# Optimization experiments

Hardware: AMD Instinct MI355X
Metric: run time of the kernel (lower is better)

The kernel has to match this reference:

```python
import jax, jax.numpy as jnp
import numpy as np

D = 256
H = 8
HD = D // H  # 32
EPS = 1e-5


def _ln(x, g, b):
    m = jnp.mean(x, axis=-1, keepdims=True)
    v = jnp.var(x, axis=-1, keepdims=True)
    return (x - m) * jax.lax.rsqrt(v + EPS) * g + b


def setup_inputs() -> dict:
    key = jax.random.key(0)
    ks = jax.random.split(key, 30)
    B = 131072
    s = 0.05

    def w(k, shape, scale=s):
        return jax.random.normal(k, shape, dtype=jnp.float32) * scale

    inp = {
        'f24': w(ks[0], (B, D), 1.0),
        'f77': w(ks[1], (B, D), 1.0),
        'fx': w(ks[2], (B, D), 1.0),
        'norm_g': jnp.ones((D,), jnp.float32),
        'norm_b': jnp.zeros((D,), jnp.float32),
        'Wq24': w(ks[3], (D, D)), 'bq24': w(ks[4], (D,)),
        'Wk24': w(ks[5], (D, D)), 'bk24': w(ks[6], (D,)),
        'Wv24': w(ks[7], (D, D)), 'bv24': w(ks[8], (D,)),
        'Wq77': w(ks[9], (D, D)), 'bq77': w(ks[10], (D,)),
        'Wk77': w(ks[11], (D, D)), 'bk77': w(ks[12], (D,)),
        'Wv77': w(ks[13], (D, D)), 'bv77': w(ks[14], (D,)),
        'Wqx': w(ks[15], (D, D)), 'bqx': w(ks[16], (D,)),
        'Wkx': w(ks[17], (D, D)), 'bkx': w(ks[18], (D,)),
        'Wvx': w(ks[19], (D, D)), 'bvx': w(ks[20], (D,)),
        'Wout': w(ks[21], (D, D)), 'bout': w(ks[22], (D,)),
        'radar_w': jnp.ones((3,), jnp.float32),
        'W1': w(ks[23], (D, 4 * D)), 'b1': w(ks[24], (4 * D,)),
        'W2': w(ks[25], (4 * D, D)), 'b2': w(ks[26], (D,)),
        'fnorm_g': jnp.ones((D,), jnp.float32),
        'fnorm_b': jnp.zeros((D,), jnp.float32),
    }
    return inp


def reference(f24, f77, fx, norm_g, norm_b,
              Wq24, bq24, Wk24, bk24, Wv24, bv24,
              Wq77, bq77, Wk77, bk77, Wv77, bv77,
              Wqx, bqx, Wkx, bkx, Wvx, bvx,
              Wout, bout, radar_w, W1, b1, W2, b2,
              fnorm_g, fnorm_b):
    B = f24.shape[0]
    residual = (f24 + f77 + fx) / 3.0
    n24 = _ln(f24, norm_g, norm_b)
    n77 = _ln(f77, norm_g, norm_b)
    nx = _ln(fx, norm_g, norm_b)

    def proj(x, W, b):
        return (x @ W + b).reshape(B, H, HD)

    q24 = proj(n24, Wq24, bq24); k24 = proj(n24, Wk24, bk24); v24 = proj(n24, Wv24, bv24)
    q77 = proj(n77, Wq77, bq77); k77 = proj(n77, Wk77, bk77); v77 = proj(n77, Wv77, bv77)
    qx = proj(nx, Wqx, bqx); kx = proj(nx, Wkx, bkx); vx = proj(nx, Wvx, bvx)

    scale = HD ** (-0.5)

    def att(q, ka, kb):  # [B,H,H] each
        a = jnp.einsum('bhd,bgd->bhg', q, ka) * scale
        b_ = jnp.einsum('bhd,bgd->bhg', q, kb) * scale
        # softmax across the two radar sources (stacked dim), NOT over keys
        return jax.nn.softmax(jnp.stack([a, b_], axis=1), axis=1)

    attn_24 = att(q24, k77, kx)
    attn_77 = att(q77, k24, kx)
    attn_x = att(qx, k24, k77)

    def mix(p, va, vb):  # [B,2,H,H] x [B,H,HD] -> [B, D]
        o = jnp.einsum('bhg,bgd->bhd', p[:, 0], va) + jnp.einsum('bhg,bgd->bhd', p[:, 1], vb)
        return o.reshape(B, D)

    out_24 = mix(attn_24, v77, vx)
    out_77 = mix(attn_77, v24, vx)
    out_x = mix(attn_x, v24, v77)

    rw = jax.nn.softmax(radar_w, axis=0)
    fused = rw[0] * out_24 + rw[1] * out_77 + rw[2] * out_x
    fused = fused @ Wout + bout
    fused = fused + residual
    ff = jax.nn.gelu(fused @ W1 + b1, approximate=False) @ W2 + b2  # dropout = eval identity
    output = _ln(fused + ff, fnorm_g, fnorm_b)
    return output, rw
```

## Files before the change

kernel.cpp:

```cpp
#include <hip/hip_runtime.h>

#define DEV __device__ __forceinline__

typedef float f4_t __attribute__((ext_vector_type(4)));
typedef short v8s  __attribute__((ext_vector_type(8)));

DEV float lo16(unsigned int w){ return __uint_as_float(w << 16); }
DEV float hi16(unsigned int w){ return __uint_as_float(w & 0xffff0000u); }
DEV float b2f(unsigned short u){ return __uint_as_float((unsigned)u << 16); }
DEV unsigned short f2b(float f){
  unsigned int x = __float_as_uint(f);
  x += 0x7fffu + ((x >> 16) & 1u);
  return (unsigned short)(x >> 16);
}
DEV float geluf(float v){ return 0.5f * v * (1.0f + erff(v * 0.7071067811865475f)); }

DEV void gload_lds16(const unsigned short* g, unsigned short* l){
  __builtin_amdgcn_global_load_lds(
      (const __attribute__((address_space(1))) void*)g,
      (__attribute__((address_space(3))) void*)l, 16, 0, 0);
}

#define WAITV(n) asm volatile("s_waitcnt vmcnt(" #n ")" ::: "memory")
#define SBAR()  do{ __builtin_amdgcn_sched_barrier(0); \
                    asm volatile("s_barrier" ::: "memory"); \
                    __builtin_amdgcn_sched_barrier(0); }while(0)

__global__ void k_prep(
    const float* Wq24, const float* Wk24, const float* Wv24,
    const float* Wq77, const float* Wk77, const float* Wv77,
    const float* Wqx,  const float* Wkx,  const float* Wvx,
    const float* bq24, const float* bk24, const float* bv24,
    const float* bq77, const float* bk77, const float* bv77,
    const float* bqx,  const float* bkx,  const float* bvx,
    const float* Wout, const float* W1,   const float* W2,
    const float* radar_w,
    unsigned short* wt_cat, unsigned short* wout_t,
    unsigned short* w1_t, unsigned short* w2_t,
    float* bias_cat, float* rwbuf, float* out_tail)
{
  long idx = (long)blockIdx.x * blockDim.x + threadIdx.x;
  if (idx < 589824){
    int s = (int)(idx / 196608);
    int r = (int)(idx % 196608);
    int ng = r >> 8, k = r & 255;
    int which = ng >> 8, n = ng & 255;
    const float* src;
    switch (s*3 + which){
      case 0: src = Wq24; break;  case 1: src = Wk24; break;  case 2: src = Wv24; break;
      case 3: src = Wq77; break;  case 4: src = Wk77; break;  case 5: src = Wv77; break;
      case 6: src = Wqx;  break;  case 7: src = Wkx;  break;  default: src = Wvx; break;
    }
    wt_cat[idx] = f2b(src[k*256 + n]);
    return;
  }
  idx -= 589824;
  if (idx < 65536){ int n = (int)(idx >> 8), k = (int)(idx & 255);
    wout_t[idx] = f2b(Wout[k*256 + n]); return; }
  idx -= 65536;
  if (idx < 262144){ int n = (int)(idx >> 8), k = (int)(idx & 255);
    w1_t[idx] = f2b(W1[k*1024 + n]); return; }
  idx -= 262144;
  if (idx < 262144){ int n = (int)(idx >> 10), k = (int)(idx & 1023);
    w2_t[idx] = f2b(W2[k*256 + n]); return; }
  idx -= 262144;
  if (idx < 2304){
    int s = (int)(idx / 768), j = (int)(idx % 768);
    int which = j >> 8, jj = j & 255;
    const float* src;
    switch (s*3 + which){
      case 0: src = bq24; break;  case 1: src = bk24; break;  case 2: src = bv24; break;
      case 3: src = bq77; break;  case 4: src = bk77; break;  case 5: src = bv77; break;
      case 6: src = bqx;  break;  case 7: src = bkx;  break;  default: src = bvx; break;
    }
    bias_cat[idx] = src[jj]; return;
  }
  idx -= 2304;
  if (idx < 3){
    float w0 = radar_w[0], w1v = radar_w[1], w2v = radar_w[2];
    float m = fmaxf(w0, fmaxf(w1v, w2v));
    float e0 = __expf(w0-m), e1 = __expf(w1v-m), e2 = __expf(w2v-m);
    float inv = 1.0f/(e0+e1+e2);
    float rw = (idx==0 ? e0 : (idx==1 ? e1 : e2)) * inv;
    rwbuf[idx] = rw; out_tail[idx] = rw;
  }
}

__global__ __launch_bounds__(256) void k_ln3(
    const float* __restrict__ f24, const float* __restrict__ f77, const float* __restrict__ fx,
    const float* __restrict__ gg, const float* __restrict__ bb,
    unsigned short* __restrict__ nbuf, float* __restrict__ resid, int rows)
{
  int wid = threadIdx.x >> 6, lane = threadIdx.x & 63;
  long row = (long)blockIdx.x*4 + wid;
  long base = row*256 + lane*4;
  f4_t x0 = *(const f4_t*)(f24 + base);
  f4_t x1 = *(const f4_t*)(f77 + base);
  f4_t x2 = *(const f4_t*)(fx  + base);
  float s[3], q[3];
  s[0]=x0.x+x0.y+x0.z+x0.w;
  s[1]=x1.x+x1.y+x1.z+x1.w;
  s[2]=x2.x+x2.y+x2.z+x2.w;
  q[0]=fmaf(x0.x,x0.x,fmaf(x0.y,x0.y,fmaf(x0.z,x0.z,x0.w*x0.w)));
  q[1]=fmaf(x1.x,x1.x,fmaf(x1.y,x1.y,fmaf(x1.z,x1.z,x1.w*x1.w)));
  q[2]=fmaf(x2.x,x2.x,fmaf(x2.y,x2.y,fmaf(x2.z,x2.z,x2.w*x2.w)));
  #pragma unroll
  for (int m=1;m<64;m<<=1){
    #pragma unroll
    for (int j=0;j<3;j++){ s[j]+=__shfl_xor(s[j],m); q[j]+=__shfl_xor(q[j],m); }
  }
  f4_t G  = *(const f4_t*)(gg + lane*4);
  f4_t Bv = *(const f4_t*)(bb + lane*4);
  long strm = (long)rows*256;
  {
    float mean = s[0]*(1.0f/256.0f);
    float rstd = rsqrtf(q[0]*(1.0f/256.0f) - mean*mean + 1e-5f);
    ushort4 o;
    o.x=f2b((x0.x-mean)*rstd*G.x+Bv.x); o.y=f2b((x0.y-mean)*rstd*G.y+Bv.y);
    o.z=f2b((x0.z-mean)*rstd*G.z+Bv.z); o.w=f2b((x0.w-mean)*rstd*G.w+Bv.w);
    *(ushort4*)(nbuf + base) = o;
  }
  {
    float mean = s[1]*(1.0f/256.0f);
    float rstd = rsqrtf(q[1]*(1.0f/256.0f) - mean*mean + 1e-5f);
    ushort4 o;
    o.x=f2b((x1.x-mean)*rstd*G.x+Bv.x); o.y=f2b((x1.y-mean)*rstd*G.y+Bv.y);
    o.z=f2b((x1.z-mean)*rstd*G.z+Bv.z); o.w=f2b((x1.w-mean)*rstd*G.w+Bv.w);
    *(ushort4*)(nbuf + strm + base) = o;
  }
  {
    float mean = s[2]*(1.0f/256.0f);
    float rstd = rsqrtf(q[2]*(1.0f/256.0f) - mean*mean + 1e-5f);
    ushort4 o;
    o.x=f2b((x2.x-mean)*rstd*G.x+Bv.x); o.y=f2b((x2.y-mean)*rstd*G.y+Bv.y);
    o.z=f2b((x2.z-mean)*rstd*G.z+Bv.z); o.w=f2b((x2.w-mean)*rstd*G.w+Bv.w);
    *(ushort4*)(nbuf + 2*strm + base) = o;
  }
  f4_t rs;
  rs.x=(x0.x+x1.x+x2.x)*(1.0f/3.0f);
  rs.y=(x0.y+x1.y+x2.y)*(1.0f/3.0f);
  rs.z=(x0.z+x1.z+x2.z)*(1.0f/3.0f);
  rs.w=(x0.w+x1.w+x2.w)*(1.0f/3.0f);
  *(f4_t*)(resid + base) = rs;
}

template<int EPI>
__global__ __launch_bounds__(256,2) void k_gemm256(
    const unsigned short* __restrict__ A, const unsigned short* __restrict__ Bt,
    const float* __restrict__ bias, const float* __restrict__ resid,
    unsigned short* __restrict__ outH,
    long aBatch, long bBatch, long biasBatch, long oBatch, int ldOut,
    int tM, int tN, int tZ)
{
  __shared__ __align__(16) unsigned short As[2][128][64];
  __shared__ __align__(16) unsigned short Bs[2][128][64];
  int tid = threadIdx.x, wid = tid >> 6, lane = tid & 63;
  int wm = (wid >> 1)*64, wn = (wid & 1)*64;
  int lr = lane & 15, lk = lane >> 4;

  int total = tM*tN*tZ;
  int nT = (total - (int)blockIdx.x + (int)gridDim.x - 1) / (int)gridDim.x;
  if (nT <= 0) return;
  int G = nT*4;

  auto tileOf = [&](int j, long& m0, int& n0, int& z){
    int T = (int)blockIdx.x + j*(int)gridDim.x;
    int mt = T % tM; int rest = T / tM;
    int nt = rest % tN; z = rest / tN;
    m0 = (long)mt*128; n0 = nt*128;
  };

  auto stage = [&](int g){
    long m0; int n0, z;
    tileOf(g >> 2, m0, n0, z);
    int k0 = (g & 3)*64, bi = g & 1;
    const unsigned short* Ab = A  + (long)z*aBatch + m0*256;
    const unsigned short* Bb = Bt + (long)z*bBatch + (long)n0*256;
    #pragma unroll
    for (int i=0;i<4;i++){
      int c = (wid*4+i)*64 + lane;
      int r = c >> 3, sl = (c & 7) ^ (r & 7);
      gload_lds16(Ab + (long)r*256 + k0 + sl*8, &As[bi][0][0] + (long)(wid*4+i)*512);
      gload_lds16(Bb + (long)r*256 + k0 + sl*8, &Bs[bi][0][0] + (long)(wid*4+i)*512);
    }
  };

  const f4_t fz = {0.f,0.f,0.f,0.f};
  f4_t acc[4][4] = {};

  stage(0);
  for (int g=0; g<G; ++g){
    if (g+1 < G){ stage(g+1); WAITV(8); }
    else        { WAITV(0); }
    SBAR();
    int cur = g & 1;
    #pragma unroll
    for (int ks=0; ks<2; ++ks){
      v8s af[4], bfv[4];
      #pragma unroll
      for (int f=0; f<4; f++){
        int prA = wm + f*16 + lr;
        int prB = wn + f*16 + lr;
        int js  = ks*4 + lk;
        af[f]  = *(const v8s*)&As[cur][prA][(js ^ (prA & 7))*8];
        bfv[f] = *(const v8s*)&Bs[cur][prB][(js ^ (prB & 7))*8];
      }
      #pragma unroll
      for (int fm=0; fm<4; fm++)
        #pragma unroll
        for (int fn=0; fn<4; fn++)
          acc[fm][fn] = __builtin_amdgcn_mfma_f32_16x16x32_bf16(bfv[fn], af[fm], acc[fm][fn], 0,0,0);
    }
    if ((g & 3) == 3){
      long m0; int n0, z;
      tileOf(g >> 2, m0, n0, z);
      long zo = (long)z*oBatch;
      const float* bp = bias + (long)z*biasBatch;
      #pragma unroll
      for (int fm=0; fm<4; fm++){
        long gm = m0 + wm + fm*16 + lr;
        long rowo = zo + gm*(long)ldOut;
        #pragma unroll
        for (int fn=0; fn<4; fn++){
          int gn = n0 + wn + fn*16 + lk*4;
          f4_t bv = *(const f4_t*)(bp + gn);
          f4_t v = acc[fm][fn];
          v.x += bv.x; v.y += bv.y; v.z += bv.z; v.w += bv.w;
          if (EPI == 1){
            f4_t rv = *(const f4_t*)(resid + rowo + gn);
            v.x += rv.x; v.y += rv.y; v.z += rv.z; v.w += rv.w;
          }
          if (EPI == 2){ v.x=geluf(v.x); v.y=geluf(v.y); v.z=geluf(v.z); v.w=geluf(v.w); }
          ushort4 o; o.x=f2b(v.x); o.y=f2b(v.y); o.z=f2b(v.z); o.w=f2b(v.w);
          *(ushort4*)(outH + rowo + gn) = o;
          acc[fm][fn] = fz;
        }
      }
    }
    SBAR();
  }
}

__global__ __launch_bounds__(512,4) void k_attn(
    const unsigned short* __restrict__ qkv, const float* __restrict__ rwb,
    unsigned short* __restrict__ outA, int rows)
{
  __shared__ __align__(16) unsigned short L[8][72][40];
  int tid = threadIdx.x, wid = tid >> 6, lane = tid & 63;
  long brow0 = (long)blockIdx.x * 8;
  for (int c = tid; c < 2304; c += 512){
    int row = c / 288, rem = c % 288;
    int s = rem / 96, cc = rem % 96;
    int vi = cc >> 2, ch = cc & 3;
    const uint4* src = (const uint4*)(qkv + ((long)s*rows + brow0 + row)*768 + cc*8);
    *(uint4*)&L[row][s*24 + vi][ch*8] = *src;
  }
  __syncthreads();

  int h = lane >> 3, g = lane & 7;
  const unsigned short* R = &L[wid][0][0];
  float comb[32];
  #pragma unroll
  for (int i=0;i<32;i++) comb[i] = 0.0f;
  float rw0 = rwb[0], rw1 = rwb[1], rw2 = rwb[2];

  #pragma unroll
  for (int att=0; att<3; ++att){
    int qs  = att;
    int as_ = (att==0) ? 1 : 0;
    int bs_ = (att==2) ? 1 : 2;
    float rwv = (att==0) ? rw0 : ((att==1) ? rw1 : rw2);
    const unsigned short* qp  = R + (qs *24      + h)*40;
    const unsigned short* kap = R + (as_*24 + 8  + g)*40;
    const unsigned short* kbp = R + (bs_*24 + 8  + g)*40;
    float a = 0.0f, b = 0.0f;
    #pragma unroll
    for (int j=0;j<4;j++){
      uint4 qc  = *(const uint4*)(qp  + j*8);
      uint4 kac = *(const uint4*)(kap + j*8);
      uint4 kbc = *(const uint4*)(kbp + j*8);
      #define DOT2(QW,KA,KB) { float q0=lo16(QW), q1=hi16(QW); \
        a=fmaf(q0,lo16(KA),a); a=fmaf(q1,hi16(KA),a); \
        b=fmaf(q0,lo16(KB),b); b=fmaf(q1,hi16(KB),b); }
      DOT2(qc.x, kac.x, kbc.x) DOT2(qc.y, kac.y, kbc.y)
      DOT2(qc.z, kac.z, kbc.z) DOT2(qc.w, kac.w, kbc.w)
      #undef DOT2
    }
    float d  = (b - a) * 0.17677669529663689f;
    float p0 = 1.0f / (1.0f + __expf(d));
    float p1 = 1.0f - p0;
    float w0 = rwv * p0, w1 = rwv * p1;
    const unsigned short* vap = R + (as_*24 + 16 + g)*40;
    const unsigned short* vbp = R + (bs_*24 + 16 + g)*40;
    #pragma unroll
    for (int j=0;j<4;j++){
      uint4 va = *(const uint4*)(vap + j*8);
      uint4 vb = *(const uint4*)(vbp + j*8);
      #define MIX2(VA,VB,C0,C1) { \
        C0 = fmaf(w0, lo16(VA), fmaf(w1, lo16(VB), C0)); \
        C1 = fmaf(w0, hi16(VA), fmaf(w1, hi16(VB), C1)); }
      MIX2(va.x, vb.x, comb[j*8+0], comb[j*8+1])
      MIX2(va.y, vb.y, comb[j*8+2], comb[j*8+3])
      MIX2(va.z, vb.z, comb[j*8+4], comb[j*8+5])
      MIX2(va.w, vb.w, comb[j*8+6], comb[j*8+7])
      #undef MIX2
    }
  }

  float t16[16];
  { bool up = (lane & 4) != 0;
    #pragma unroll
    for (int i=0;i<16;i++){
      float send = up ? comb[i] : comb[16+i];
      float keep = up ? comb[16+i] : comb[i];
      t16[i] = keep + __shfl_xor(send, 4);
    } }
  float t8[8];
  { bool up = (lane & 2) != 0;
    #pragma unroll
    for (int i=0;i<8;i++){
      float send = up ? t16[i] : t16[8+i];
      float keep = up ? t16[8+i] : t16[i];
      t8[i] = keep + __shfl_xor(send, 2);
    } }
  float t4[4];
  { bool up = (lane & 1) != 0;
    #pragma unroll
    for (int i=0;i<4;i++){
      float send = up ? t8[i] : t8[4+i];
      float keep = up ? t8[4+i] : t8[i];
      t4[i] = keep + __shfl_xor(send, 1);
    } }

  long orow = brow0 + wid;
  ushort4 o4;
  o4.x = f2b(t4[0]); o4.y = f2b(t4[1]); o4.z = f2b(t4[2]); o4.w = f2b(t4[3]);
  *(ushort4*)(outA + orow*256 + lane*4) = o4;
}

__global__ __launch_bounds__(512,4) void k_ff2ln(
    const unsigned short* __restrict__ A, const unsigned short* __restrict__ Bt,
    const float* __restrict__ b2, const unsigned short* __restrict__ fusedH,
    const float* __restrict__ fg, const float* __restrict__ fb,
    float* __restrict__ dout)
{
  __shared__ __align__(16) union {
    struct { unsigned short As[2][64][64]; unsigned short Bs[2][256][64]; } st;
    float rowbuf[64][264];
  } u;
  int tid = threadIdx.x, wid = tid >> 6, lane = tid & 63;
  long m0 = (long)blockIdx.x * 64;
  const unsigned short* Ab = A + m0*1024;

  auto stage = [&](int it){
    int k0 = (it)*64, bi = it & 1;
    { int c = wid*64 + lane; int r = c >> 3, sl = (c & 7) ^ (r & 7);
      gload_lds16(Ab + (long)r*1024 + k0 + sl*8, &u.st.As[bi][0][0] + (long)wid*512); }
    #pragma unroll
    for (int i=0;i<4;i++){
      int j = wid*4 + i; int c = j*64 + lane; int r = c >> 3, sl = (c & 7) ^ (r & 7);
      gload_lds16(Bt + (long)r*1024 + k0 + sl*8, &u.st.Bs[bi][0][0] + (long)j*512);
    }
  };

  f4_t acc[2][4] = {};
  int wm = (wid >> 2)*32, wn = (wid & 3)*64;
  int lr = lane & 15, lk = lane >> 4;

  stage(0);
  for (int it=0; it<16; ++it){
    if (it+1 < 16){ stage(it+1); WAITV(5); }
    else          { WAITV(0); }
    SBAR();
    int cur = it & 1;
    #pragma unroll
    for (int ks=0; ks<2; ++ks){
      v8s af[2], bfv[4];
      #pragma unroll
      for (int f=0; f<2; f++){
        int pr = wm + f*16 + lr;
        af[f]  = *(const v8s*)&u.st.As[cur][pr][((ks*4+lk) ^ (pr & 7))*8];
      }
      #pragma unroll
      for (int f=0; f<4; f++){
        int pr = wn + f*16 + lr;
        bfv[f] = *(const v8s*)&u.st.Bs[cur][pr][((ks*4+lk) ^ (pr & 7))*8];
      }
      #pragma unroll
      for (int fm=0; fm<2; fm++)
        #pragma unroll
        for (int fn=0; fn<4; fn++)
          acc[fm][fn] = __builtin_amdgcn_mfma_f32_16x16x32_bf16(bfv[fn], af[fm], acc[fm][fn], 0,0,0);
    }
    SBAR();
  }

  #pragma unroll
  for (int fm=0; fm<2; fm++){
    int rl = wm + fm*16 + lr;
    #pragma unroll
    for (int fn=0; fn<4; fn++){
      int cl = wn + fn*16 + lk*4;
      f4_t bv = *(const f4_t*)(b2 + cl);
      ushort4 fh = *(const ushort4*)(fusedH + (m0 + rl)*256 + cl);
      f4_t v = acc[fm][fn];
      v.x += bv.x + b2f(fh.x);
      v.y += bv.y + b2f(fh.y);
      v.z += bv.z + b2f(fh.z);
      v.w += bv.w + b2f(fh.w);
      *(f4_t*)&u.rowbuf[rl][cl] = v;
    }
  }
  __syncthreads();

  f4_t G  = *(const f4_t*)(fg + lane*4);
  f4_t Bv = *(const f4_t*)(fb + lane*4);
  #pragma unroll
  for (int rr=0; rr<8; ++rr){
    int row = wid*8 + rr;
    f4_t x = *(const f4_t*)&u.rowbuf[row][lane*4];
    float s = x.x + x.y + x.z + x.w;
    float q = fmaf(x.x,x.x, fmaf(x.y,x.y, fmaf(x.z,x.z, x.w*x.w)));
    #pragma unroll
    for (int m=1;m<64;m<<=1){ s += __shfl_xor(s,m); q += __shfl_xor(q,m); }
    float mean = s*(1.0f/256.0f);
    float rstd = rsqrtf(q*(1.0f/256.0f) - mean*mean + 1e-5f);
    f4_t o;
    o.x = (x.x-mean)*rstd*G.x + Bv.x;
    o.y = (x.y-mean)*rstd*G.y + Bv.y;
    o.z = (x.z-mean)*rstd*G.z + Bv.z;
    o.w = (x.w-mean)*rstd*G.w + Bv.w;
    *(f4_t*)(dout + (m0 + row)*256 + lane*4) = o;
  }
}

extern "C" void kernel_launch(void* const* d_in, const int* in_sizes, int n_in,
                              void* d_out, int out_size, void* d_ws, size_t ws_size,
                              hipStream_t stream)
{
  const float* f24    = (const float*)d_in[0];
  const float* f77    = (const float*)d_in[1];
  const float* fx     = (const float*)d_in[2];
  const float* norm_g = (const float*)d_in[3];
  const float* norm_b = (const float*)d_in[4];
  const float* Wq24 = (const float*)d_in[5];  const float* bq24 = (const float*)d_in[6];
  const float* Wk24 = (const float*)d_in[7];  const float* bk24 = (const float*)d_in[8];
  const float* Wv24 = (const float*)d_in[9];  const float* bv24 = (const float*)d_in[10];
  const float* Wq77 = (const float*)d_in[11]; const float* bq77 = (const float*)d_in[12];
  const float* Wk77 = (const float*)d_in[13]; const float* bk77 = (const float*)d_in[14];
  const float* Wv77 = (const float*)d_in[15]; const float* bv77 = (const float*)d_in[16];
  const float* Wqx  = (const float*)d_in[17]; const float* bqx  = (const float*)d_in[18];
  const float* Wkx  = (const float*)d_in[19]; const float* bkx  = (const float*)d_in[20];
  const float* Wvx  = (const float*)d_in[21]; const float* bvx  = (const float*)d_in[22];
  const float* Wout = (const float*)d_in[23]; const float* bout = (const float*)d_in[24];
  const float* radar_w = (const float*)d_in[25];
  const float* W1 = (const float*)d_in[26];   const float* b1 = (const float*)d_in[27];
  const float* W2 = (const float*)d_in[28];   const float* b2 = (const float*)d_in[29];
  const float* fnorm_g = (const float*)d_in[30];
  const float* fnorm_b = (const float*)d_in[31];

  const long Brows = (long)in_sizes[0] / 256;
  float* dout = (float*)d_out;
  char* ws = (char*)d_ws;

  size_t off = 0;
  auto A_ = [&](size_t b){ size_t o = off; off = (off + b + 255) & ~(size_t)255; return o; };
  size_t oWT = A_((size_t)3*768*256*2);
  size_t oWO = A_((size_t)65536*2);
  size_t oW1 = A_((size_t)262144*2);
  size_t oW2 = A_((size_t)262144*2);
  size_t oBC = A_((size_t)2304*4);
  size_t oRW = A_(256);
  size_t fixedEnd = off;

  unsigned short* WT_CAT = (unsigned short*)(ws + oWT);
  unsigned short* WOUT_T = (unsigned short*)(ws + oWO);
  unsigned short* W1_T   = (unsigned short*)(ws + oW1);
  unsigned short* W2_T   = (unsigned short*)(ws + oW2);
  float*          BIASC  = (float*)(ws + oBC);
  float*          RW     = (float*)(ws + oRW);

  const size_t PER_ROW = 7168;
  if (ws_size <= fixedEnd + 512) return;
  long maxR = (long)((ws_size - fixedEnd - 256) / PER_ROW);
  maxR &= ~127L;
  if (maxR < 128) return;
  long Rc = maxR < 16384 ? maxR : 16384;
  if (Rc > Brows) Rc = Brows;
  long nch = (Brows + Rc - 1) / Rc;
  Rc = ((Brows + nch - 1) / nch + 127) & ~127L;

  size_t chunkBase = (fixedEnd + 255) & ~(size_t)255;
  char* NB_B = ws + chunkBase;
  char* RS_B = NB_B + (size_t)1536*Rc;
  char* QK_B = RS_B + (size_t)1024*Rc;

  {
    long total = 589824 + 65536 + 262144 + 262144 + 2304 + 3;
    int blocks = (int)((total + 255) / 256);
    k_prep<<<blocks, 256, 0, stream>>>(
        Wq24, Wk24, Wv24, Wq77, Wk77, Wv77, Wqx, Wkx, Wvx,
        bq24, bk24, bv24, bq77, bk77, bv77, bqx, bkx, bvx,
        Wout, W1, W2, radar_w,
        WT_CAT, WOUT_T, W1_T, W2_T, BIASC, RW, dout + (size_t)Brows*256);
  }

  for (long row0 = 0; row0 < Brows; row0 += Rc){
    long rows = Brows - row0 < Rc ? Brows - row0 : Rc;
    unsigned short* NBUF   = (unsigned short*)NB_B;
    float*          RESID  = (float*)RS_B;
    unsigned short* QKV    = (unsigned short*)QK_B;
    unsigned short* ATTN   = (unsigned short*)NB_B;
    unsigned short* FUSEDH = (unsigned short*)QK_B;
    unsigned short* HBUF   = (unsigned short*)(QK_B + (size_t)rows*256*2);

    int tM = (int)(rows/128);

    k_ln3<<<(int)(rows/4), 256, 0, stream>>>(
        f24 + row0*256, f77 + row0*256, fx + row0*256,
        norm_g, norm_b, NBUF, RESID, (int)rows);

    { int tiles = tM*6*3; int grid = tiles < 512 ? tiles : 512;
      k_gemm256<0><<<grid, 256, 0, stream>>>(
          NBUF, WT_CAT, BIASC, nullptr, QKV,
          rows*256L, 768L*256, 768L, rows*768L, 768, tM, 6, 3); }

    k_attn<<<(int)(rows/8), 512, 0, stream>>>(QKV, RW, ATTN, (int)rows);

    { int tiles = tM*2; int grid = tiles < 512 ? tiles : 512;
      k_gemm256<1><<<grid, 256, 0, stream>>>(
          ATTN, WOUT_T, bout, RESID, FUSEDH,
          0, 0, 0, 0, 256, tM, 2, 1); }

    { int tiles = tM*8; int grid = tiles < 512 ? tiles : 512;
      k_gemm256<2><<<grid, 256, 0, stream>>>(
          FUSEDH, W1_T, b1, nullptr, HBUF,
          0, 0, 0, 0, 1024, tM, 8, 1); }

    k_ff2ln<<<(int)(rows/64), 512, 0, stream>>>(
        HBUF, W2_T, b2, FUSEDH, fnorm_g, fnorm_b, dout + row0*256);
  }
}
```

Baseline: 1.445 ms.

## Replace persistent GEMM tile loop with one-tile-per-block grid and shrink attention blocks

The GEMM kernel no longer loops persistently over tiles with cross-tile prefetch. Each block now computes a single 128x128 tile from a 3D grid, with the bias hoisted ahead of the K loop and the 4-step K loop fully unrolled. The attention kernel moves from 512-thread blocks handling 8 rows to 256-thread blocks handling 4 rows, with a higher occupancy hint. This cuts index arithmetic and lets the hardware scheduler balance work across CUs, but it gives up prefetching the next tile during the epilogue and adds launch overhead from many more blocks.

After: 1.989 ms. 1.38x slower.

```diff
diff --git a/kernel.cpp b/kernel.cpp
--- a/kernel.cpp
+++ b/kernel.cpp
@@ -149,33 +149,21 @@
     const unsigned short* __restrict__ A, const unsigned short* __restrict__ Bt,
     const float* __restrict__ bias, const float* __restrict__ resid,
     unsigned short* __restrict__ outH,
-    long aBatch, long bBatch, long biasBatch, long oBatch, int ldOut,
-    int tM, int tN, int tZ)
+    long aBatch, long bBatch, long biasBatch, long oBatch, int ldOut)
 {
   __shared__ __align__(16) unsigned short As[2][128][64];
   __shared__ __align__(16) unsigned short Bs[2][128][64];
   int tid = threadIdx.x, wid = tid >> 6, lane = tid & 63;
   int wm = (wid >> 1)*64, wn = (wid & 1)*64;
   int lr = lane & 15, lk = lane >> 4;
-
-  int total = tM*tN*tZ;
-  int nT = (total - (int)blockIdx.x + (int)gridDim.x - 1) / (int)gridDim.x;
-  if (nT <= 0) return;
-  int G = nT*4;
-
-  auto tileOf = [&](int j, long& m0, int& n0, int& z){
-    int T = (int)blockIdx.x + j*(int)gridDim.x;
-    int mt = T % tM; int rest = T / tM;
-    int nt = rest % tN; z = rest / tN;
-    m0 = (long)mt*128; n0 = nt*128;
-  };
-
-  auto stage = [&](int g){
-    long m0; int n0, z;
-    tileOf(g >> 2, m0, n0, z);
-    int k0 = (g & 3)*64, bi = g & 1;
-    const unsigned short* Ab = A  + (long)z*aBatch + m0*256;
-    const unsigned short* Bb = Bt + (long)z*bBatch + (long)n0*256;
+  long m0 = (long)blockIdx.x * 128;
+  int  n0 = blockIdx.y * 128;
+  int  z  = blockIdx.z;
+  const unsigned short* Ab = A  + (long)z*aBatch + m0*256;
+  const unsigned short* Bb = Bt + (long)z*bBatch + (long)n0*256;
+
+  auto stage = [&](int s){
+    int k0 = s*64, bi = s & 1;
     #pragma unroll
     for (int i=0;i<4;i++){
       int c = (wid*4+i)*64 + lane;
@@ -185,15 +173,19 @@
     }
   };
 
-  const f4_t fz = {0.f,0.f,0.f,0.f};
+  const float* bp = bias + (long)z*biasBatch;
+  f4_t bv[4];
+  #pragma unroll
+  for (int fn=0; fn<4; fn++) bv[fn] = *(const f4_t*)(bp + n0 + wn + fn*16 + lk*4);
+
   f4_t acc[4][4] = {};
-
   stage(0);
-  for (int g=0; g<G; ++g){
-    if (g+1 < G){ stage(g+1); WAITV(8); }
-    else        { WAITV(0); }
+  #pragma unroll
+  for (int s=0; s<4; ++s){
+    if (s < 3){ stage(s+1); WAITV(8); }
+    else      { WAITV(0); }
     SBAR();
-    int cur = g & 1;
+    int cur = s & 1;
     #pragma unroll
     for (int ks=0; ks<2; ++ks){
       v8s af[4], bfv[4];
@@ -211,44 +203,38 @@
         for (int fn=0; fn<4; fn++)
           acc[fm][fn] = __builtin_amdgcn_mfma_f32_16x16x32_bf16(bfv[fn], af[fm], acc[fm][fn], 0,0,0);
     }
-    if ((g & 3) == 3){
-      long m0; int n0, z;
-      tileOf(g >> 2, m0, n0, z);
-      long zo = (long)z*oBatch;
-      const float* bp = bias + (long)z*biasBatch;
-      #pragma unroll
-      for (int fm=0; fm<4; fm++){
-        long gm = m0 + wm + fm*16 + lr;
-        long rowo = zo + gm*(long)ldOut;
-        #pragma unroll
-        for (int fn=0; fn<4; fn++){
-          int gn = n0 + wn + fn*16 + lk*4;
-          f4_t bv = *(const f4_t*)(bp + gn);
-          f4_t v = acc[fm][fn];
-          v.x += bv.x; v.y += bv.y; v.z += bv.z; v.w += bv.w;
-          if (EPI == 1){
-            f4_t rv = *(const f4_t*)(resid + rowo + gn);
-            v.x += rv.x; v.y += rv.y; v.z += rv.z; v.w += rv.w;
-          }
-          if (EPI == 2){ v.x=geluf(v.x); v.y=geluf(v.y); v.z=geluf(v.z); v.w=geluf(v.w); }
-          ushort4 o; o.x=f2b(v.x); o.y=f2b(v.y); o.z=f2b(v.z); o.w=f2b(v.w);
-          *(ushort4*)(outH + rowo + gn) = o;
-          acc[fm][fn] = fz;
-        }
+    if (s < 3) SBAR();
+  }
+
+  long zo = (long)z*oBatch;
+  #pragma unroll
+  for (int fm=0; fm<4; fm++){
+    long gm = m0 + wm + fm*16 + lr;
+    long rowo = zo + gm*(long)ldOut;
+    #pragma unroll
+    for (int fn=0; fn<4; fn++){
+      int gn = n0 + wn + fn*16 + lk*4;
+      f4_t v = acc[fm][fn];
+      v.x += bv[fn].x; v.y += bv[fn].y; v.z += bv[fn].z; v.w += bv[fn].w;
+      if (EPI == 1){
+        f4_t rv = *(const f4_t*)(resid + rowo + gn);
+        v.x += rv.x; v.y += rv.y; v.z += rv.z; v.w += rv.w;
       }
-    }
-    SBAR();
-  }
-}
-
-__global__ __launch_bounds__(512,4) void k_attn(
+      if (EPI == 2){ v.x=geluf(v.x); v.y=geluf(v.y); v.z=geluf(v.z); v.w=geluf(v.w); }
+      ushort4 o; o.x=f2b(v.x); o.y=f2b(v.y); o.z=f2b(v.z); o.w=f2b(v.w);
+      *(ushort4*)(outH + rowo + gn) = o;
+    }
+  }
+}
+
+__global__ __launch_bounds__(256,6) void k_attn(
     const unsigned short* __restrict__ qkv, const float* __restrict__ rwb,
     unsigned short* __restrict__ outA, int rows)
 {
-  __shared__ __align__(16) unsigned short L[8][72][40];
+  __shared__ __align__(16) unsigned short L[4][72][40];
   int tid = threadIdx.x, wid = tid >> 6, lane = tid & 63;
-  long brow0 = (long)blockIdx.x * 8;
-  for (int c = tid; c < 2304; c += 512){
+  long brow0 = (long)blockIdx.x * 4;
+  for (int c = tid; c < 1152; c += 256){
     int row = c / 288, rem = c % 288;
     int s = rem / 96, cc = rem % 96;
     int vi = cc >> 2, ch = cc & 3;
@@ -520,22 +506,19 @@
         f24 + row0*256, f77 + row0*256, fx + row0*256,
         norm_g, norm_b, NBUF, RESID, (int)rows);
 
-    { int tiles = tM*6*3; int grid = tiles < 512 ? tiles : 512;
-      k_gemm256<0><<<grid, 256, 0, stream>>>(
-          NBUF, WT_CAT, BIASC, nullptr, QKV,
-          rows*256L, 768L*256, 768L, rows*768L, 768, tM, 6, 3); }
-
-    k_attn<<<(int)(rows/8), 512, 0, stream>>>(QKV, RW, ATTN, (int)rows);
-
-    { int tiles = tM*2; int grid = tiles < 512 ? tiles : 512;
-      k_gemm256<1><<<grid, 256, 0, stream>>>(
-          ATTN, WOUT_T, bout, RESID, FUSEDH,
-          0, 0, 0, 0, 256, tM, 2, 1); }
-
-    { int tiles = tM*8; int grid = tiles < 512 ? tiles : 512;
-      k_gemm256<2><<<grid, 256, 0, stream>>>(
-          FUSEDH, W1_T, b1, nullptr, HBUF,
-          0, 0, 0, 0, 1024, tM, 8, 1); }
+    k_gemm256<0><<<dim3(tM, 6, 3), 256, 0, stream>>>(
+        NBUF, WT_CAT, BIASC, nullptr, QKV,
+        rows*256L, 768L*256, 768L, rows*768L, 768);
+
+    k_attn<<<(int)(rows/4), 256, 0, stream>>>(QKV, RW, ATTN, (int)rows);
+
+    k_gemm256<1><<<dim3(tM, 2, 1), 256, 0, stream>>>(
+        ATTN, WOUT_T, bout, RESID, FUSEDH,
+        0, 0, 0, 0, 256);
+
+    k_gemm256<2><<<dim3(tM, 8, 1), 256, 0, stream>>>(
+        FUSEDH, W1_T, b1, nullptr, HBUF,
+        0, 0, 0, 0, 1024);
 
     k_ff2ln<<<(int)(rows/64), 512, 0, stream>>>(
         HBUF, W2_T, b2, FUSEDH, fnorm_g, fnorm_b, dout + row0*256);
```

## Fuse out-projection, FFN and final LayerNorm into one per-row-block kernel

Applied to the files above, without the earlier changes.

Replaces the separate Wout GEMM, W1+GELU GEMM and W2+LayerNorm kernel with a single kernel that processes 32 rows per block. It keeps the fused activations and the GELU hidden slices in LDS, so the FUSEDH and 1024-wide HBUF intermediates never travel through global memory. It also raises the chunk size cap so fewer chunks are launched. The trade-off is that each block re-streams the full Wout, W1 and W2 weights from L2 with no double buffering and many __syncthreads, and the M-tile is small (32 rows), which lowers MFMA reuse.

Result: slower. 1.613 ms (+11.7%).

```diff
diff --git a/kernel.cpp b/kernel.cpp
--- a/kernel.cpp
+++ b/kernel.cpp
@@ -147,7 +147,7 @@
 template<int EPI>
 __global__ __launch_bounds__(256,2) void k_gemm256(
     const unsigned short* __restrict__ A, const unsigned short* __restrict__ Bt,
-    const float* __restrict__ bias, const float* __restrict__ resid,
+    const float* __restrict__ bias,
     unsigned short* __restrict__ outH,
     long aBatch, long bBatch, long biasBatch, long oBatch, int ldOut,
     int tM, int tN, int tZ)
@@ -226,11 +226,6 @@
           f4_t bv = *(const f4_t*)(bp + gn);
           f4_t v = acc[fm][fn];
           v.x += bv.x; v.y += bv.y; v.z += bv.z; v.w += bv.w;
-          if (EPI == 1){
-            f4_t rv = *(const f4_t*)(resid + rowo + gn);
-            v.x += rv.x; v.y += rv.y; v.z += rv.z; v.w += rv.w;
-          }
-          if (EPI == 2){ v.x=geluf(v.x); v.y=geluf(v.y); v.z=geluf(v.z); v.w=geluf(v.w); }
           ushort4 o; o.x=f2b(v.x); o.y=f2b(v.y); o.z=f2b(v.z); o.w=f2b(v.w);
           *(ushort4*)(outH + rowo + gn) = o;
           acc[fm][fn] = fz;
@@ -338,99 +333,182 @@
   *(ushort4*)(outA + orow*256 + lane*4) = o4;
 }
 
-__global__ __launch_bounds__(512,4) void k_ff2ln(
-    const unsigned short* __restrict__ A, const unsigned short* __restrict__ Bt,
-    const float* __restrict__ b2, const unsigned short* __restrict__ fusedH,
+__global__ __launch_bounds__(256,2) void k_back(
+    const unsigned short* __restrict__ attn,
+    const float* __restrict__ resid,
+    const unsigned short* __restrict__ woutT,
+    const unsigned short* __restrict__ w1T,
+    const unsigned short* __restrict__ w2T,
+    const float* __restrict__ bout, const float* __restrict__ b1,
+    const float* __restrict__ b2,
     const float* __restrict__ fg, const float* __restrict__ fb,
     float* __restrict__ dout)
 {
-  __shared__ __align__(16) union {
-    struct { unsigned short As[2][64][64]; unsigned short Bs[2][256][64]; } st;
-    float rowbuf[64][264];
-  } u;
+  __shared__ __align__(16) unsigned short FL[8192];
+  __shared__ __align__(16) unsigned short STG[16384];
+  __shared__ __align__(16) unsigned short R2[4096];
   int tid = threadIdx.x, wid = tid >> 6, lane = tid & 63;
-  long m0 = (long)blockIdx.x * 64;
-  const unsigned short* Ab = A + m0*1024;
-
-  auto stage = [&](int it){
-    int k0 = (it)*64, bi = it & 1;
-    { int c = wid*64 + lane; int r = c >> 3, sl = (c & 7) ^ (r & 7);
-      gload_lds16(Ab + (long)r*1024 + k0 + sl*8, &u.st.As[bi][0][0] + (long)wid*512); }
-    #pragma unroll
-    for (int i=0;i<4;i++){
-      int j = wid*4 + i; int c = j*64 + lane; int r = c >> 3, sl = (c & 7) ^ (r & 7);
-      gload_lds16(Bt + (long)r*1024 + k0 + sl*8, &u.st.Bs[bi][0][0] + (long)j*512);
-    }
-  };
-
-  f4_t acc[2][4] = {};
-  int wm = (wid >> 2)*32, wn = (wid & 3)*64;
   int lr = lane & 15, lk = lane >> 4;
-
-  stage(0);
-  for (int it=0; it<16; ++it){
-    if (it+1 < 16){ stage(it+1); WAITV(5); }
-    else          { WAITV(0); }
-    SBAR();
-    int cur = it & 1;
+  int wn = wid*64, wnB = wid*32;
+  long m0 = (long)blockIdx.x * 32;
+
+  f4_t accA[2][4] = {};
+  for (int t=0; t<4; ++t){
+    { int c = tid; int r = c>>3, sl = (c&7)^(r&7);
+      gload_lds16(attn + (m0+r)*256 + t*64 + sl*8, R2 + c*8); }
+    #pragma unroll
+    for (int i=0;i<8;i++){ int c = i*256+tid; int r = c>>3, sl = (c&7)^(r&7);
+      gload_lds16(woutT + (long)r*256 + t*64 + sl*8, STG + c*8); }
+    __syncthreads();
     #pragma unroll
     for (int ks=0; ks<2; ++ks){
-      v8s af[2], bfv[4];
-      #pragma unroll
-      for (int f=0; f<2; f++){
-        int pr = wm + f*16 + lr;
-        af[f]  = *(const v8s*)&u.st.As[cur][pr][((ks*4+lk) ^ (pr & 7))*8];
-      }
-      #pragma unroll
-      for (int f=0; f<4; f++){
-        int pr = wn + f*16 + lr;
-        bfv[f] = *(const v8s*)&u.st.Bs[cur][pr][((ks*4+lk) ^ (pr & 7))*8];
-      }
+      v8s af[2], bf[4];
+      #pragma unroll
+      for (int f=0; f<2; f++){ int pr = f*16+lr;
+        af[f] = *(const v8s*)(R2 + pr*64 + (((ks*4+lk) ^ (pr&7))*8)); }
+      #pragma unroll
+      for (int f=0; f<4; f++){ int pr = wn + f*16 + lr;
+        bf[f] = *(const v8s*)(STG + pr*64 + (((ks*4+lk) ^ (pr&7))*8)); }
       #pragma unroll
       for (int fm=0; fm<2; fm++)
         #pragma unroll
         for (int fn=0; fn<4; fn++)
-          acc[fm][fn] = __builtin_amdgcn_mfma_f32_16x16x32_bf16(bfv[fn], af[fm], acc[fm][fn], 0,0,0);
-    }
-    SBAR();
-  }
-
+          accA[fm][fn] = __builtin_amdgcn_mfma_f32_16x16x32_bf16(bf[fn], af[fm], accA[fm][fn], 0,0,0);
+    }
+    __syncthreads();
+  }
   #pragma unroll
   for (int fm=0; fm<2; fm++){
-    int rl = wm + fm*16 + lr;
+    int row = fm*16 + lr;
     #pragma unroll
     for (int fn=0; fn<4; fn++){
-      int cl = wn + fn*16 + lk*4;
-      f4_t bv = *(const f4_t*)(b2 + cl);
-      ushort4 fh = *(const ushort4*)(fusedH + (m0 + rl)*256 + cl);
-      f4_t v = acc[fm][fn];
-      v.x += bv.x + b2f(fh.x);
-      v.y += bv.y + b2f(fh.y);
-      v.z += bv.z + b2f(fh.z);
-      v.w += bv.w + b2f(fh.w);
-      *(f4_t*)&u.rowbuf[rl][cl] = v;
+      int col = wn + fn*16 + lk*4;
+      f4_t bv = *(const f4_t*)(bout + col);
+      f4_t rv = *(const f4_t*)(resid + (m0+row)*256 + col);
+      f4_t v = accA[fm][fn];
+      v.x += bv.x + rv.x; v.y += bv.y + rv.y; v.z += bv.z + rv.z; v.w += bv.w + rv.w;
+      ushort4 hh; hh.x=f2b(v.x); hh.y=f2b(v.y); hh.z=f2b(v.z); hh.w=f2b(v.w);
+      int us = row*256 + (((col>>3) ^ (row&7))*8) + (col&7);
+      *(ushort4*)(FL + us) = hh;
     }
   }
   __syncthreads();
 
-  f4_t G  = *(const f4_t*)(fg + lane*4);
-  f4_t Bv = *(const f4_t*)(fb + lane*4);
+  f4_t acc2[2][4] = {};
+  for (int s=0; s<8; ++s){
+    f4_t accH[2][2] = {};
+    for (int t=0; t<4; ++t){
+      #pragma unroll
+      for (int i=0;i<4;i++){ int c = i*256+tid; int r = c>>3, sl = (c&7)^(r&7);
+        gload_lds16(w1T + (long)(s*128+r)*256 + t*64 + sl*8, STG + c*8); }
+      __syncthreads();
+      #pragma unroll
+      for (int ks=0; ks<2; ++ks){
+        v8s af[2], bf[2];
+        #pragma unroll
+        for (int f=0; f<2; f++){ int pr = f*16+lr; int ku = t*8 + ks*4 + lk;
+          af[f] = *(const v8s*)(FL + pr*256 + ((ku ^ (pr&7))*8)); }
+        #pragma unroll
+        for (int f=0; f<2; f++){ int pr = wnB + f*16 + lr;
+          bf[f] = *(const v8s*)(STG + pr*64 + (((ks*4+lk) ^ (pr&7))*8)); }
+        #pragma unroll
+        for (int fm=0; fm<2; fm++)
+          #pragma unroll
+          for (int fn=0; fn<2; fn++)
+            accH[fm][fn] = __builtin_amdgcn_mfma_f32_16x16x32_bf16(bf[fn], af[fm], accH[fm][fn], 0,0,0);
+      }
+      __syncthreads();
+    }
+    #pragma unroll
+    for (int fm=0; fm<2; fm++){
+      int row = fm*16 + lr;
+      #pragma unroll
+      for (int fn=0; fn<2; fn++){
+        int col = wnB + fn*16 + lk*4;
+        f4_t bv = *(const f4_t*)(b1 + s*128 + col);
+        f4_t v = accH[fm][fn];
+        v.x = geluf(v.x+bv.x); v.y = geluf(v.y+bv.y);
+        v.z = geluf(v.z+bv.z); v.w = geluf(v.w+bv.w);
+        ushort4 hh; hh.x=f2b(v.x); hh.y=f2b(v.y); hh.z=f2b(v.z); hh.w=f2b(v.w);
+        int us = row*128 + (((col>>3) ^ (row&7))*8) + (col&7);
+        *(ushort4*)(R2 + us) = hh;
+      }
+    }
+    __syncthreads();
+    for (int t=0; t<2; ++t){
+      #pragma unroll
+      for (int i=0;i<8;i++){ int c = i*256+tid; int r = c>>3, sl = (c&7)^(r&7);
+        gload_lds16(w2T + (long)r*1024 + s*128 + t*64 + sl*8, STG + c*8); }
+      __syncthreads();
+      #pragma unroll
+      for (int ks=0; ks<2; ++ks){
+        v8s af[2], bf[4];
+        #pragma unroll
+        for (int f=0; f<2; f++){ int pr = f*16+lr; int ku = t*8 + ks*4 + lk;
+          af[f] = *(const v8s*)(R2 + pr*128 + ((ku ^ (pr&7))*8)); }
+        #pragma unroll
+        for (int f=0; f<4; f++){ int pr = wn + f*16 + lr;
+          bf[f] = *(const v8s*)(STG + pr*64 + (((ks*4+lk) ^ (pr&7))*8)); }
+        #pragma unroll
+        for (int fm=0; fm<2; fm++)
+          #pragma unroll
+          for (int fn=0; fn<4; fn++)
+            acc2[fm][fn] = __builtin_amdgcn_mfma_f32_16x16x32_bf16(bf[fn], af[fm], acc2[fm][fn], 0,0,0);
+      }
+      __syncthreads();
+    }
+  }
+
+  f4_t vv[2][4];
+  float ps[2], pq[2];
   #pragma unroll
-  for (int rr=0; rr<8; ++rr){
-    int row = wid*8 + rr;
-    f4_t x = *(const f4_t*)&u.rowbuf[row][lane*4];
-    float s = x.x + x.y + x.z + x.w;
-    float q = fmaf(x.x,x.x, fmaf(x.y,x.y, fmaf(x.z,x.z, x.w*x.w)));
-    #pragma unroll
-    for (int m=1;m<64;m<<=1){ s += __shfl_xor(s,m); q += __shfl_xor(q,m); }
-    float mean = s*(1.0f/256.0f);
-    float rstd = rsqrtf(q*(1.0f/256.0f) - mean*mean + 1e-5f);
-    f4_t o;
-    o.x = (x.x-mean)*rstd*G.x + Bv.x;
-    o.y = (x.y-mean)*rstd*G.y + Bv.y;
-    o.z = (x.z-mean)*rstd*G.z + Bv.z;
-    o.w = (x.w-mean)*rstd*G.w + Bv.w;
-    *(f4_t*)(dout + (m0 + row)*256 + lane*4) = o;
+  for (int fm=0; fm<2; fm++){
+    int row = fm*16 + lr;
+    ps[fm] = 0.0f; pq[fm] = 0.0f;
+    #pragma unroll
+    for (int fn=0; fn<4; fn++){
+      int col = wn + fn*16 + lk*4;
+      f4_t bv = *(const f4_t*)(b2 + col);
+      int us = row*256 + (((col>>3) ^ (row&7))*8) + (col&7);
+      ushort4 fh = *(const ushort4*)(FL + us);
+      f4_t v = acc2[fm][fn];
+      v.x += bv.x + b2f(fh.x); v.y += bv.y + b2f(fh.y);
+      v.z += bv.z + b2f(fh.z); v.w += bv.w + b2f(fh.w);
+      vv[fm][fn] = v;
+      ps[fm] += v.x+v.y+v.z+v.w;
+      pq[fm] += v.x*v.x + v.y*v.y + v.z*v.z + v.w*v.w;
+    }
+    ps[fm] += __shfl_xor(ps[fm], 16); ps[fm] += __shfl_xor(ps[fm], 32);
+    pq[fm] += __shfl_xor(pq[fm], 16); pq[fm] += __shfl_xor(pq[fm], 32);
+  }
+  float* PS = (float*)R2;
+  float* PQ = (float*)R2 + 128;
+  if (lk == 0){
+    #pragma unroll
+    for (int fm=0; fm<2; fm++){ int row = fm*16+lr;
+      PS[row*4 + wid] = ps[fm]; PQ[row*4 + wid] = pq[fm]; }
+  }
+  __syncthreads();
+  #pragma unroll
+  for (int fm=0; fm<2; fm++){
+    int row = fm*16 + lr;
+    f4_t sv = *(const f4_t*)(PS + row*4);
+    f4_t qv = *(const f4_t*)(PQ + row*4);
+    float S = sv.x+sv.y+sv.z+sv.w, Q = qv.x+qv.y+qv.z+qv.w;
+    float mean = S*(1.0f/256.0f);
+    float rstd = rsqrtf(Q*(1.0f/256.0f) - mean*mean + 1e-5f);
+    #pragma unroll
+    for (int fn=0; fn<4; fn++){
+      int col = wn + fn*16 + lk*4;
+      f4_t G = *(const f4_t*)(fg + col);
+      f4_t Bb = *(const f4_t*)(fb + col);
+      f4_t v = vv[fm][fn], o;
+      o.x = (v.x-mean)*rstd*G.x + Bb.x;
+      o.y = (v.y-mean)*rstd*G.y + Bb.y;
+      o.z = (v.z-mean)*rstd*G.z + Bb.z;
+      o.w = (v.w-mean)*rstd*G.w + Bb.w;
+      *(f4_t*)(dout + (m0+row)*256 + col) = o;
+    }
   }
 }
 
@@ -485,7 +563,7 @@
   long maxR = (long)((ws_size - fixedEnd - 256) / PER_ROW);
   maxR &= ~127L;
   if (maxR < 128) return;
-  long Rc = maxR < 16384 ? maxR : 16384;
+  long Rc = maxR < 65536 ? maxR : 65536;
   if (Rc > Brows) Rc = Brows;
   long nch = (Brows + Rc - 1) / Rc;
   Rc = ((Brows + nch - 1) / nch + 127) & ~127L;
@@ -511,8 +589,6 @@
     float*          RESID  = (float*)RS_B;
     unsigned short* QKV    = (unsigned short*)QK_B;
     unsigned short* ATTN   = (unsigned short*)NB_B;
-    unsigned short* FUSEDH = (unsigned short*)QK_B;
-    unsigned short* HBUF   = (unsigned short*)(QK_B + (size_t)rows*256*2);
 
     int tM = (int)(rows/128);
 
@@ -522,22 +598,13 @@
 
     { int tiles = tM*6*3; int grid = tiles < 512 ? tiles : 512;
       k_gemm256<0><<<grid, 256, 0, stream>>>(
-          NBUF, WT_CAT, BIASC, nullptr, QKV,
+          NBUF, WT_CAT, BIASC, QKV,
           rows*256L, 768L*256, 768L, rows*768L, 768, tM, 6, 3); }
 
     k_attn<<<(int)(rows/8), 512, 0, stream>>>(QKV, RW, ATTN, (int)rows);
 
-    { int tiles = tM*2; int grid = tiles < 512 ? tiles : 512;
-      k_gemm256<1><<<grid, 256, 0, stream>>>(
-          ATTN, WOUT_T, bout, RESID, FUSEDH,
-          0, 0, 0, 0, 256, tM, 2, 1); }
-
-    { int tiles = tM*8; int grid = tiles < 512 ? tiles : 512;
-      k_gemm256<2><<<grid, 256, 0, stream>>>(
-          FUSEDH, W1_T, b1, nullptr, HBUF,
-          0, 0, 0, 0, 1024, tM, 8, 1); }
-
-    k_ff2ln<<<(int)(rows/64), 512, 0, stream>>>(
-        HBUF, W2_T, b2, FUSEDH, fnorm_g, fnorm_b, dout + row0*256);
-  }
-}
+    k_back<<<(int)(rows/32), 256, 0, stream>>>(
+        ATTN, RESID, WOUT_T, W1_T, W2_T,
+        bout, b1, b2, fnorm_g, fnorm_b, dout + row0*256);
+  }
+}
```
